# Kernel optimization log

Hardware: AMD Instinct MI355X
Metric: run time of the kernel (lower is better)

Reference implementation:

```python
import jax, jax.numpy as jnp
import numpy as np

N = 50000      # nodes
E = 800000     # edges (avg degree 16)
D = 3          # dim_world
L = 128        # latent_dim
STEPS = 10     # message passing steps
RID = 64       # num_rigid_ids
REMB = 16      # rigid_embedding_dim


def _mlp2(x, w1, b1, w2, b2):
    # 2-layer MLP: Linear -> ReLU -> Linear (layer_norm=False, dropout=0)
    return jnp.maximum(x @ w1 + b1, 0.0) @ w2 + b2


def setup_inputs() -> dict:
    key = jax.random.key(0)
    ks = jax.random.split(key, 24)
    f32 = jnp.float32

    def lin(k, i, o):
        return (jax.random.normal(k, (i, o), f32) / np.sqrt(i)).astype(f32)

    node_in = 2 * D + 1 + REMB   # 23
    edge_in = 2 * D + 2 + 1      # 9

    receivers = jax.random.randint(ks[4], (E,), 0, N)
    # no self edges (radius_graph uses include_self_edges=False)
    senders = (receivers + jax.random.randint(ks[3], (E,), 1, N)) % N

    inp = {
        'positions': jax.random.uniform(ks[0], (N, D), f32),
        'velocities': jax.random.normal(ks[1], (N, D), f32),
        'rigid_id': jax.random.randint(ks[2], (N,), 0, RID),
        'senders': senders,
        'receivers': receivers,
        'rigid_emb': jax.random.normal(ks[5], (RID, REMB), f32) * 0.1,
        # node encoder
        'ne_w1': lin(ks[6], node_in, L), 'ne_b1': jnp.zeros((L,), f32),
        'ne_w2': lin(ks[7], L, L),       'ne_b2': jnp.zeros((L,), f32),
        # edge encoder
        'ee_w1': lin(ks[8], edge_in, L), 'ee_b1': jnp.zeros((L,), f32),
        'ee_w2': lin(ks[9], L, L),       'ee_b2': jnp.zeros((L,), f32),
        # processor blocks (stacked over STEPS)
        'pe_w1': (jax.random.normal(ks[10], (STEPS, 3 * L, L), f32) / np.sqrt(3 * L)).astype(f32),
        'pe_b1': jnp.zeros((STEPS, L), f32),
        'pe_w2': (jax.random.normal(ks[11], (STEPS, L, L), f32) / np.sqrt(L)).astype(f32),
        'pe_b2': jnp.zeros((STEPS, L), f32),
        'pn_w1': (jax.random.normal(ks[12], (STEPS, 2 * L, L), f32) / np.sqrt(2 * L)).astype(f32),
        'pn_b1': jnp.zeros((STEPS, L), f32),
        'pn_w2': (jax.random.normal(ks[13], (STEPS, L, L), f32) / np.sqrt(L)).astype(f32),
        'pn_b2': jnp.zeros((STEPS, L), f32),
        # decoder (2 layers -> output_dim = D)
        'de_w1': lin(ks[14], L, L), 'de_b1': jnp.zeros((L,), f32),
        'de_w2': lin(ks[15], L, D), 'de_b2': jnp.zeros((D,), f32),
    }
    return inp


def reference(positions, velocities, rigid_id, senders, receivers, rigid_emb,
              ne_w1, ne_b1, ne_w2, ne_b2, ee_w1, ee_b1, ee_w2, ee_b2,
              pe_w1, pe_b1, pe_w2, pe_b2, pn_w1, pn_b1, pn_w2, pn_b2,
              de_w1, de_b1, de_w2, de_b2):
    n = positions.shape[0]
    dt = positions.dtype

    # ----- feature construction (build_gns_graph_inputs + rigid features) -----
    deg = jax.ops.segment_sum(jnp.ones(receivers.shape, dt), receivers, num_segments=n)[:, None]
    center = positions.mean(axis=0, keepdims=True)
    rigid_feat = rigid_emb[rigid_id]                                # [N, REMB]
    node_feat = jnp.concatenate([velocities, positions - center, deg, rigid_feat], axis=-1)

    rel_pos = positions[senders] - positions[receivers]             # [E, D]
    rel_vel = velocities[senders] - velocities[receivers]
    sq = jnp.sum(rel_pos * rel_pos, axis=-1, keepdims=True)
    dist = jnp.sqrt(sq)
    same = (rigid_id[senders] == rigid_id[receivers]).astype(dt)[:, None]
    edge_feat = jnp.concatenate([rel_pos, rel_vel, dist, sq, same], axis=-1)

    # ----- encode -----
    nl = _mlp2(node_feat, ne_w1, ne_b1, ne_w2, ne_b2)               # [N, L]
    el = _mlp2(edge_feat, ee_w1, ee_b1, ee_w2, ee_b2)               # [E, L]

    # ----- process: gather -> edge MLP -> scatter-add -> node MLP, residual -----
    for i in range(pe_w1.shape[0]):
        edge_in = jnp.concatenate([el, nl[senders], nl[receivers]], axis=-1)  # [E, 3L]
        el = el + _mlp2(edge_in, pe_w1[i], pe_b1[i], pe_w2[i], pe_b2[i])
        agg = jax.ops.segment_sum(el, receivers, num_segments=n)              # [N, L]
        node_in = jnp.concatenate([nl, agg], axis=-1)                         # [N, 2L]
        nl = nl + _mlp2(node_in, pn_w1[i], pn_b1[i], pn_w2[i], pn_b2[i])

    # ----- decode -----
    return _mlp2(nl, de_w1, de_b1, de_w2, de_b2)                    # [N, D]
```

## Files before the change

### kernel.cpp

```cpp
#include <hip/hip_runtime.h>
#include <hip/hip_bf16.h>

#define NN 50000
#define NE 800000
#define LDIM 128
#define NSTEPS 10

typedef __hip_bfloat16 bf16;
typedef __bf16 bf8v __attribute__((ext_vector_type(8)));
typedef float f4v __attribute__((ext_vector_type(4)));
typedef unsigned short u16x8 __attribute__((ext_vector_type(8)));

__device__ inline float bflo(unsigned int u) {
    union { unsigned int i; float f; } x; x.i = u << 16; return x.f;
}
__device__ inline float bfhi(unsigned int u) {
    union { unsigned int i; float f; } x; x.i = u & 0xffff0000u; return x.f;
}
__device__ inline unsigned short f2bf(float f) {
    __hip_bfloat16 h = __float2bfloat16(f);
    unsigned short u; __builtin_memcpy(&u, &h, 2); return u;
}

__device__ __forceinline__ void gl_lds16(const void* g, void* l) {
    __builtin_amdgcn_global_load_lds(
        (const __attribute__((address_space(1))) unsigned int*)g,
        (__attribute__((address_space(3))) unsigned int*)l, 16, 0, 0);
}


__global__ void k_hist(const int* __restrict__ rcv, int* __restrict__ cnt) {
    int i = blockIdx.x * 256 + threadIdx.x;
    if (i < NE) atomicAdd(&cnt[rcv[i]], 1);
}

__global__ __launch_bounds__(1024) void k_scan(
    const int* __restrict__ cnt, int* __restrict__ row_start,
    int* __restrict__ cur, float* __restrict__ degf) {
    __shared__ int part[1024];
    const int t = threadIdx.x;
    const int CH = (NN + 1023) / 1024;
    int b0 = t * CH, b1 = b0 + CH; if (b1 > NN) b1 = NN; if (b0 > NN) b0 = NN;
    int s = 0;
    for (int i = b0; i < b1; i++) s += cnt[i];
    part[t] = s;
    __syncthreads();
    for (int off = 1; off < 1024; off <<= 1) {
        int v = (t >= off) ? part[t - off] : 0;
        __syncthreads();
        part[t] += v;
        __syncthreads();
    }
    int run = part[t] - s;
    for (int i = b0; i < b1; i++) {
        row_start[i] = run; cur[i] = run; degf[i] = (float)cnt[i];
        run += cnt[i];
    }
    if (t == 1023) row_start[NN] = part[1023];
}

__global__ void k_scatter(const int* __restrict__ snd, const int* __restrict__ rcv,
                          int* __restrict__ cur,
                          unsigned short* __restrict__ snd_p, unsigned short* __restrict__ rcv_p) {
    int i = blockIdx.x * 256 + threadIdx.x;
    if (i < NE) {
        int r = rcv[i];
        int p = atomicAdd(&cur[r], 1);
        snd_p[p] = (unsigned short)snd[i];
        rcv_p[p] = (unsigned short)r;
    }
}

__global__ void k_center(const float* __restrict__ pos, float* __restrict__ csum) {
    __shared__ float s[3][256];
    float a = 0.f, b = 0.f, c = 0.f;
    for (int i = blockIdx.x * 256 + threadIdx.x; i < NN; i += gridDim.x * 256) {
        a += pos[3 * i]; b += pos[3 * i + 1]; c += pos[3 * i + 2];
    }
    int t = threadIdx.x;
    s[0][t] = a; s[1][t] = b; s[2][t] = c;
    __syncthreads();
    for (int off = 128; off > 0; off >>= 1) {
        if (t < off) {
            s[0][t] += s[0][t + off];
            s[1][t] += s[1][t + off];
            s[2][t] += s[2][t + off];
        }
        __syncthreads();
    }
    if (t == 0) {
        atomicAdd(&csum[0], s[0][0]);
        atomicAdd(&csum[1], s[1][0]);
        atomicAdd(&csum[2], s[2][0]);
    }
}


__global__ void k_prep_w(const float* __restrict__ w, unsigned short* __restrict__ wf,
                         int KT, int Ksrc, int lo) {
    int b = blockIdx.x;
    int s = b / (KT * 8), rem = b % (KT * 8);
    int kt = rem / 8, nt = rem % 8;
    int lane = threadIdx.x, col = lane & 15, quad = lane >> 4;
    const float* W = w + (size_t)s * Ksrc * 128;
    u16x8 o;
#pragma unroll
    for (int jj = 0; jj < 8; jj++) {
        int k = kt * 32 + quad * 8 + jj;
        float x = (k < Ksrc) ? W[(size_t)k * 128 + nt * 16 + col] : 0.f;
        unsigned short h = f2bf(x);
        if (lo) h = f2bf(x - bflo(h));
        o[jj] = h;
    }
    *(u16x8*)(wf + (((size_t)b) * 64 + lane) * 8) = o;
}


__global__ __launch_bounds__(256) void k_agg(
    const unsigned short* __restrict__ el, const int* __restrict__ row_start,
    unsigned short* __restrict__ agg) {
    const int wave = threadIdx.x >> 6, lane = threadIdx.x & 63;
    const int n = blockIdx.x * 4 + wave;
    if (n >= NN) return;
    const int sub = lane >> 4, c16 = lane & 15;
    const int st = row_start[n], en = row_start[n + 1];
    float s[8];
#pragma unroll
    for (int k = 0; k < 8; k++) s[k] = 0.f;
    for (int q = st + sub; q < en; q += 4) {
        uint4 v = *(const uint4*)(el + (size_t)q * 128 + c16 * 8);
        s[0] += bflo(v.x); s[1] += bfhi(v.x);
        s[2] += bflo(v.y); s[3] += bfhi(v.y);
        s[4] += bflo(v.z); s[5] += bfhi(v.z);
        s[6] += bflo(v.w); s[7] += bfhi(v.w);
    }
#pragma unroll
    for (int k = 0; k < 8; k++) {
        s[k] += __shfl_xor(s[k], 16);
        s[k] += __shfl_xor(s[k], 32);
    }
    if (sub == 0) {
        u16x8 o;
#pragma unroll
        for (int k = 0; k < 8; k++) o[k] = f2bf(s[k]);
        *(u16x8*)(agg + (size_t)n * 128 + c16 * 8) = o;
    }
}


__global__ __launch_bounds__(256) void k_node_enc_m(
    const float* __restrict__ pos, const float* __restrict__ vel,
    const int* __restrict__ rid, const float* __restrict__ remb,
    const float* __restrict__ degf, const float* __restrict__ csum,
    const unsigned short* __restrict__ w1h, const unsigned short* __restrict__ w1l,
    const float* __restrict__ b1,
    const unsigned short* __restrict__ w2h, const unsigned short* __restrict__ w2l,
    const float* __restrict__ b2,
    unsigned short* __restrict__ nlh, unsigned short* __restrict__ nll) {
    __shared__ __align__(16) unsigned short feat_s[32 * 72];
    __shared__ __align__(16) unsigned short hid_s[32 * 264];
    const int tid = threadIdx.x, wave = tid >> 6, lane = tid & 63;
    const int col = lane & 15, quad = lane >> 4;
    bf8v W1H[2], W1L[2], W2H[4][2], W2L[4][2];
#pragma unroll
    for (int t = 0; t < 2; t++) {
        W1H[t] = *(const bf8v*)(w1h + ((size_t)(2 * wave + t) * 64 + lane) * 8);
        W1L[t] = *(const bf8v*)(w1l + ((size_t)(2 * wave + t) * 64 + lane) * 8);
    }
#pragma unroll
    for (int kt = 0; kt < 4; kt++)
#pragma unroll
        for (int t = 0; t < 2; t++) {
            W2H[kt][t] = *(const bf8v*)(w2h + ((size_t)(kt * 8 + 2 * wave + t) * 64 + lane) * 8);
            W2L[kt][t] = *(const bf8v*)(w2l + ((size_t)(kt * 8 + 2 * wave + t) * 64 + lane) * 8);
        }
    float bias1[2], bias2[2];
#pragma unroll
    for (int t = 0; t < 2; t++) {
        bias1[t] = b1[(2 * wave + t) * 16 + col];
        bias2[t] = b2[(2 * wave + t) * 16 + col];
    }
    float cx = csum[0] * (1.0f / NN), cy = csum[1] * (1.0f / NN), cz = csum[2] * (1.0f / NN);
    uint4 z = {0u, 0u, 0u, 0u};
    for (int s2 = tid; s2 < 288; s2 += 256) *(uint4*)(feat_s + s2 * 8) = z;

    for (int it = 0; it < 4; it++) {
        const int base = blockIdx.x * 128 + it * 32;
        if (base >= NN) break;
        __syncthreads();
        if (tid < 32) {
            int n = base + tid; if (n > NN - 1) n = NN - 1;
            float v[23];
            v[0] = vel[3 * n]; v[1] = vel[3 * n + 1]; v[2] = vel[3 * n + 2];
            v[3] = pos[3 * n] - cx; v[4] = pos[3 * n + 1] - cy; v[5] = pos[3 * n + 2] - cz;
            v[6] = degf[n];
            int rb = rid[n] * 16;
#pragma unroll
            for (int k = 0; k < 16; k++) v[7 + k] = remb[rb + k];
            unsigned short* f = feat_s + tid * 72;
#pragma unroll
            for (int k = 0; k < 23; k++) {
                unsigned short h = f2bf(v[k]);
                f[k] = h; f[32 + k] = f2bf(v[k] - bflo(h));
            }
        }
        __syncthreads();
        f4v acc[2][2];
#pragma unroll
        for (int mt = 0; mt < 2; mt++)
#pragma unroll
            for (int t = 0; t < 2; t++) acc[mt][t] = (f4v){0.f, 0.f, 0.f, 0.f};
        {
            bf8v a0h = *(const bf8v*)(feat_s + col * 72 + quad * 8);
            bf8v a1h = *(const bf8v*)(feat_s + (16 + col) * 72 + quad * 8);
            bf8v a0l = *(const bf8v*)(feat_s + col * 72 + 32 + quad * 8);
            bf8v a1l = *(const bf8v*)(feat_s + (16 + col) * 72 + 32 + quad * 8);
#pragma unroll
            for (int t = 0; t < 2; t++) {
                acc[0][t] = __builtin_amdgcn_mfma_f32_16x16x32_bf16(a0h, W1H[t], acc[0][t], 0, 0, 0);
                acc[1][t] = __builtin_amdgcn_mfma_f32_16x16x32_bf16(a1h, W1H[t], acc[1][t], 0, 0, 0);
                acc[0][t] = __builtin_amdgcn_mfma_f32_16x16x32_bf16(a0l, W1H[t], acc[0][t], 0, 0, 0);
                acc[1][t] = __builtin_amdgcn_mfma_f32_16x16x32_bf16(a1l, W1H[t], acc[1][t], 0, 0, 0);
                acc[0][t] = __builtin_amdgcn_mfma_f32_16x16x32_bf16(a0h, W1L[t], acc[0][t], 0, 0, 0);
                acc[1][t] = __builtin_amdgcn_mfma_f32_16x16x32_bf16(a1h, W1L[t], acc[1][t], 0, 0, 0);
            }
        }
#pragma unroll
        for (int mt = 0; mt < 2; mt++)
#pragma unroll
// ... 121 lines not shown
        f4v acc[2][2];
#pragma unroll
        for (int mt = 0; mt < 2; mt++)
#pragma unroll
            for (int t = 0; t < 2; t++) acc[mt][t] = (f4v){0.f, 0.f, 0.f, 0.f};
        {
            bf8v a0h = *(const bf8v*)(feat_s + col * 72 + quad * 8);
            bf8v a1h = *(const bf8v*)(feat_s + (16 + col) * 72 + quad * 8);
            bf8v a0l = *(const bf8v*)(feat_s + col * 72 + 32 + quad * 8);
            bf8v a1l = *(const bf8v*)(feat_s + (16 + col) * 72 + 32 + quad * 8);
#pragma unroll
            for (int t = 0; t < 2; t++) {
                acc[0][t] = __builtin_amdgcn_mfma_f32_16x16x32_bf16(a0h, W1H[t], acc[0][t], 0, 0, 0);
                acc[1][t] = __builtin_amdgcn_mfma_f32_16x16x32_bf16(a1h, W1H[t], acc[1][t], 0, 0, 0);
                acc[0][t] = __builtin_amdgcn_mfma_f32_16x16x32_bf16(a0l, W1H[t], acc[0][t], 0, 0, 0);
                acc[1][t] = __builtin_amdgcn_mfma_f32_16x16x32_bf16(a1l, W1H[t], acc[1][t], 0, 0, 0);
                acc[0][t] = __builtin_amdgcn_mfma_f32_16x16x32_bf16(a0h, W1L[t], acc[0][t], 0, 0, 0);
                acc[1][t] = __builtin_amdgcn_mfma_f32_16x16x32_bf16(a1h, W1L[t], acc[1][t], 0, 0, 0);
            }
        }
#pragma unroll
        for (int mt = 0; mt < 2; mt++)
#pragma unroll
            for (int t = 0; t < 2; t++) {
                const int nc = (2 * wave + t) * 16 + col;
#pragma unroll
                for (int r = 0; r < 4; r++) {
                    float h = fmaxf(acc[mt][t][r] + bias1[t], 0.f);
                    unsigned short hh = f2bf(h);
                    hid_s[(mt * 16 + quad * 4 + r) * 264 + nc] = hh;
                    hid_s[(mt * 16 + quad * 4 + r) * 264 + 128 + nc] = f2bf(h - bflo(hh));
                }
            }
        __syncthreads();
#pragma unroll
        for (int mt = 0; mt < 2; mt++)
#pragma unroll
            for (int t = 0; t < 2; t++) acc[mt][t] = (f4v){0.f, 0.f, 0.f, 0.f};
#pragma unroll
        for (int kt = 0; kt < 8; kt++) {
            int w = kt & 3;
            bf8v a0 = *(const bf8v*)(hid_s + col * 264 + kt * 32 + quad * 8);
            bf8v a1 = *(const bf8v*)(hid_s + (16 + col) * 264 + kt * 32 + quad * 8);
#pragma unroll
            for (int t = 0; t < 2; t++) {
                acc[0][t] = __builtin_amdgcn_mfma_f32_16x16x32_bf16(a0, W2H[w][t], acc[0][t], 0, 0, 0);
                acc[1][t] = __builtin_amdgcn_mfma_f32_16x16x32_bf16(a1, W2H[w][t], acc[1][t], 0, 0, 0);
            }
        }
#pragma unroll
        for (int kt = 0; kt < 4; kt++) {
            bf8v a0 = *(const bf8v*)(hid_s + col * 264 + kt * 32 + quad * 8);
            bf8v a1 = *(const bf8v*)(hid_s + (16 + col) * 264 + kt * 32 + quad * 8);
#pragma unroll
            for (int t = 0; t < 2; t++) {
                acc[0][t] = __builtin_amdgcn_mfma_f32_16x16x32_bf16(a0, W2L[kt][t], acc[0][t], 0, 0, 0);
                acc[1][t] = __builtin_amdgcn_mfma_f32_16x16x32_bf16(a1, W2L[kt][t], acc[1][t], 0, 0, 0);
            }
        }
        __syncthreads();
#pragma unroll
        for (int mt = 0; mt < 2; mt++)
#pragma unroll
            for (int t = 0; t < 2; t++) {
                const int nc = (2 * wave + t) * 16 + col;
#pragma unroll
                for (int r = 0; r < 4; r++)
                    hid_s[(mt * 16 + quad * 4 + r) * 264 + nc] = f2bf(acc[mt][t][r] + bias2[t]);
            }
        __syncthreads();
#pragma unroll
        for (int p = 0; p < 2; p++) {
            int s2 = p * 256 + tid, e = s2 >> 4, c16 = s2 & 15;
            *(uint4*)(el + (size_t)(base + e) * 128 + c16 * 8) =
                *(const uint4*)(hid_s + e * 264 + c16 * 8);
        }
    }
}


__global__ __launch_bounds__(256) void k_edge_step(
    unsigned short* __restrict__ el, const unsigned short* __restrict__ nlh,
    const unsigned short* __restrict__ snd, const unsigned short* __restrict__ rcv,
    const unsigned short* __restrict__ w1f, const float* __restrict__ b1,
    const unsigned short* __restrict__ w2f, const float* __restrict__ b2) {
    __shared__ __align__(1024) unsigned short stage_s[2][3][32][128];
    __shared__ __align__(16) unsigned short hid_s[32 * 136];
    const int tid = threadIdx.x;
    const int wave = tid >> 6, lane = tid & 63;
    const int col = lane & 15, quad = lane >> 4;
    const int erow = tid >> 4, c16 = tid & 15;

    bf8v W1[12][2], W2[4][2];
#pragma unroll
    for (int kt = 0; kt < 12; kt++)
#pragma unroll
        for (int t = 0; t < 2; t++)
            W1[kt][t] = *(const bf8v*)(w1f + ((size_t)(kt * 8 + 2 * wave + t) * 64 + lane) * 8);
#pragma unroll
    for (int kt = 0; kt < 4; kt++)
#pragma unroll
        for (int t = 0; t < 2; t++)
            W2[kt][t] = *(const bf8v*)(w2f + ((size_t)(kt * 8 + 2 * wave + t) * 64 + lane) * 8);
    float bias1[2], bias2[2];
#pragma unroll
    for (int t = 0; t < 2; t++) {
        bias1[t] = b1[(2 * wave + t) * 16 + col];
        bias2[t] = b2[(2 * wave + t) * 16 + col];
    }

    const int srow0 = wave * 8 + (lane >> 4);
    const int srow1 = srow0 + 4;
    const int skb = (lane & 15) * 16;
    const int soff0 = skb ^ ((srow0 & 7) << 4);
    const int soff1 = skb ^ ((srow1 & 7) << 4);
    const int gb0 = blockIdx.x * 128;
    const char* elc = (const char*)el;
    const char* nlc = (const char*)nlh;

    auto issue = [&](int t, int b, int si0, int si1, int ri0, int ri1) {
        char* s0 = (char*)&stage_s[b][0][wave * 8][0];
        char* s1 = (char*)&stage_s[b][1][wave * 8][0];
        char* s2 = (char*)&stage_s[b][2][wave * 8][0];
        const size_t gb = (size_t)(gb0 + t * 32);
        gl_lds16(elc + (gb + srow0) * 256 + soff0, s0);
        gl_lds16(elc + (gb + srow1) * 256 + soff1, s0 + 1024);
        gl_lds16(nlc + (size_t)si0 * 256 + soff0, s1);
        gl_lds16(nlc + (size_t)si1 * 256 + soff1, s1 + 1024);
        gl_lds16(nlc + (size_t)ri0 * 256 + soff0, s2);
        gl_lds16(nlc + (size_t)ri1 * 256 + soff1, s2 + 1024);
    };

    {
        int si0 = snd[gb0 + srow0], si1 = snd[gb0 + srow1];
        int ri0 = rcv[gb0 + srow0], ri1 = rcv[gb0 + srow1];
        issue(0, 0, si0, si1, ri0, ri1);
    }
    int nsi0 = snd[gb0 + 32 + srow0], nsi1 = snd[gb0 + 32 + srow1];
    int nri0 = rcv[gb0 + 32 + srow0], nri1 = rcv[gb0 + 32 + srow1];

    for (int it = 0; it < 4; it++) {
        const int cur = it & 1, nxt = cur ^ 1;
        const int base = gb0 + it * 32;
        __syncthreads();
        if (it < 3) {
            issue(it + 1, nxt, nsi0, nsi1, nri0, nri1);
            if (it < 2) {
                int gb = gb0 + (it + 2) * 32;
                nsi0 = snd[gb + srow0]; nsi1 = snd[gb + srow1];
                nri0 = rcv[gb + srow0]; nri1 = rcv[gb + srow1];
            }
        }

        f4v acc[2][2];
#pragma unroll
        for (int mt = 0; mt < 2; mt++)
#pragma unroll
            for (int t = 0; t < 2; t++) acc[mt][t] = (f4v){0.f, 0.f, 0.f, 0.f};
        const int sw = (col & 7) << 4;
#pragma unroll
        for (int kt = 0; kt < 12; kt++) {
            const char* sb = (const char*)&stage_s[cur][kt >> 2][0][0];
            const int kb = (kt & 3) * 64 + quad * 16;
            bf8v a0 = *(const bf8v*)(sb + col * 256 + (kb ^ sw));
            bf8v a1 = *(const bf8v*)(sb + (16 + col) * 256 + (kb ^ sw));
            acc[0][0] = __builtin_amdgcn_mfma_f32_16x16x32_bf16(a0, W1[kt][0], acc[0][0], 0, 0, 0);
            acc[0][1] = __builtin_amdgcn_mfma_f32_16x16x32_bf16(a0, W1[kt][1], acc[0][1], 0, 0, 0);
            acc[1][0] = __builtin_amdgcn_mfma_f32_16x16x32_bf16(a1, W1[kt][0], acc[1][0], 0, 0, 0);
            acc[1][1] = __builtin_amdgcn_mfma_f32_16x16x32_bf16(a1, W1[kt][1], acc[1][1], 0, 0, 0);
        }
#pragma unroll
        for (int mt = 0; mt < 2; mt++)
#pragma unroll
            for (int t = 0; t < 2; t++) {
                const int nc = (2 * wave + t) * 16 + col;
#pragma unroll
                for (int r = 0; r < 4; r++) {
                    float v = fmaxf(acc[mt][t][r] + bias1[t], 0.f);
                    hid_s[(mt * 16 + quad * 4 + r) * 136 + nc] = f2bf(v);
                }
            }
        __syncthreads();

#pragma unroll
        for (int mt = 0; mt < 2; mt++)
#pragma unroll
            for (int t = 0; t < 2; t++) acc[mt][t] = (f4v){0.f, 0.f, 0.f, 0.f};
#pragma unroll
        for (int kt = 0; kt < 4; kt++) {
            bf8v a0 = *(const bf8v*)(hid_s + col * 136 + kt * 32 + quad * 8);
            bf8v a1 = *(const bf8v*)(hid_s + (16 + col) * 136 + kt * 32 + quad * 8);
            acc[0][0] = __builtin_amdgcn_mfma_f32_16x16x32_bf16(a0, W2[kt][0], acc[0][0], 0, 0, 0);
            acc[0][1] = __builtin_amdgcn_mfma_f32_16x16x32_bf16(a0, W2[kt][1], acc[0][1], 0, 0, 0);
            acc[1][0] = __builtin_amdgcn_mfma_f32_16x16x32_bf16(a1, W2[kt][0], acc[1][0], 0, 0, 0);
            acc[1][1] = __builtin_amdgcn_mfma_f32_16x16x32_bf16(a1, W2[kt][1], acc[1][1], 0, 0, 0);
        }
        __syncthreads();

#pragma unroll
        for (int mt = 0; mt < 2; mt++)
#pragma unroll
            for (int t = 0; t < 2; t++) {
                const int nc = (2 * wave + t) * 16 + col;
#pragma unroll
                for (int r = 0; r < 4; r++) {
                    const int row = mt * 16 + quad * 4 + r;
                    float res = bflo((unsigned int)stage_s[cur][0][row][nc ^ ((row & 7) << 3)]);
                    float v = acc[mt][t][r] + bias2[t] + res;
                    hid_s[row * 136 + nc] = f2bf(v);
                }
            }
        __syncthreads();
#pragma unroll
        for (int p = 0; p < 2; p++) {
            int e = p * 16 + erow;
            *(uint4*)(el + (size_t)(base + e) * 128 + c16 * 8) =
                *(const uint4*)(hid_s + e * 136 + c16 * 8);
        }
    }
}


__global__ __launch_bounds__(256) void k_node_step_s(
    unsigned short* __restrict__ nlh, unsigned short* __restrict__ nll,
    const unsigned short* __restrict__ agg,
    const unsigned short* __restrict__ w1h, const unsigned short* __restrict__ w1l,
    const float* __restrict__ b1,
    const unsigned short* __restrict__ w2h, const unsigned short* __restrict__ w2l,
    const float* __restrict__ b2) {
    __shared__ __align__(16) unsigned short a_s[32 * 392];
    __shared__ __align__(16) unsigned short hid_s[32 * 264];
    const int tid = threadIdx.x, wave = tid >> 6, lane = tid & 63;
    const int col = lane & 15, quad = lane >> 4;
    bf8v W1H[8][2], W1L[8][2], W2H[4][2], W2L[4][2];
#pragma unroll
    for (int kt = 0; kt < 8; kt++)
#pragma unroll
        for (int t = 0; t < 2; t++) {
            W1H[kt][t] = *(const bf8v*)(w1h + ((size_t)(kt * 8 + 2 * wave + t) * 64 + lane) * 8);
            W1L[kt][t] = *(const bf8v*)(w1l + ((size_t)(kt * 8 + 2 * wave + t) * 64 + lane) * 8);
        }
#pragma unroll
    for (int kt = 0; kt < 4; kt++)
#pragma unroll
        for (int t = 0; t < 2; t++) {
            W2H[kt][t] = *(const bf8v*)(w2h + ((size_t)(kt * 8 + 2 * wave + t) * 64 + lane) * 8);
            W2L[kt][t] = *(const bf8v*)(w2l + ((size_t)(kt * 8 + 2 * wave + t) * 64 + lane) * 8);
        }
    float bias1[2], bias2[2];
#pragma unroll
    for (int t = 0; t < 2; t++) {
        bias1[t] = b1[(2 * wave + t) * 16 + col];
        bias2[t] = b2[(2 * wave + t) * 16 + col];
    }
    for (int it = 0; it < 2; it++) {
        const int base = blockIdx.x * 64 + it * 32;
        if (base >= NN) break;
        __syncthreads();
#pragma unroll
        for (int p = 0; p < 2; p++) {
            int e = p * 16 + (tid >> 4), c16 = tid & 15;
            int n = base + e; if (n > NN - 1) n = NN - 1;
            *(uint4*)(a_s + e * 392 + c16 * 8) =
                *(const uint4*)(nlh + (size_t)n * 128 + c16 * 8);
            *(uint4*)(a_s + e * 392 + 128 + c16 * 8) =
                *(const uint4*)(nll + (size_t)n * 128 + c16 * 8);
            *(uint4*)(a_s + e * 392 + 256 + c16 * 8) =
                *(const uint4*)(agg + (size_t)n * 128 + c16 * 8);
        }
        __syncthreads();

        f4v acc[2][2];
#pragma unroll
        for (int mt = 0; mt < 2; mt++)
#pragma unroll
            for (int t = 0; t < 2; t++) acc[mt][t] = (f4v){0.f, 0.f, 0.f, 0.f};
#pragma unroll
        for (int kt = 0; kt < 8; kt++) {
            bf8v a0 = *(const bf8v*)(a_s + col * 392 + kt * 32 + quad * 8);
            bf8v a1 = *(const bf8v*)(a_s + (16 + col) * 392 + kt * 32 + quad * 8);
#pragma unroll
            for (int t = 0; t < 2; t++) {
                acc[0][t] = __builtin_amdgcn_mfma_f32_16x16x32_bf16(a0, W1H[kt & 3][t], acc[0][t], 0, 0, 0);
                acc[1][t] = __builtin_amdgcn_mfma_f32_16x16x32_bf16(a1, W1H[kt & 3][t], acc[1][t], 0, 0, 0);
            }
        }
#pragma unroll
        for (int kt = 0; kt < 4; kt++) {
            bf8v a0 = *(const bf8v*)(a_s + col * 392 + 256 + kt * 32 + quad * 8);
            bf8v a1 = *(const bf8v*)(a_s + (16 + col) * 392 + 256 + kt * 32 + quad * 8);
#pragma unroll
            for (int t = 0; t < 2; t++) {
                acc[0][t] = __builtin_amdgcn_mfma_f32_16x16x32_bf16(a0, W1H[4 + kt][t], acc[0][t], 0, 0, 0);
                acc[1][t] = __builtin_amdgcn_mfma_f32_16x16x32_bf16(a1, W1H[4 + kt][t], acc[1][t], 0, 0, 0);
            }
        }
#pragma unroll
        for (int kt = 0; kt < 4; kt++) {
            bf8v a0 = *(const bf8v*)(a_s + col * 392 + kt * 32 + quad * 8);
            bf8v a1 = *(const bf8v*)(a_s + (16 + col) * 392 + kt * 32 + quad * 8);
#pragma unroll
// ... 103 lines not shown
        float w[8];
#pragma unroll
        for (int t = 0; t < 8; t++) w[t] = w1[(kc * 8 + t) * 128 + j];
#pragma unroll
        for (int e = 0; e < 16; e++) {
            float4 h0 = *(const float4*)&inl[e][kc * 8];
            float4 h1 = *(const float4*)&inl[e][kc * 8 + 4];
            acc[e] = fmaf(h0.x, w[0], acc[e]); acc[e] = fmaf(h0.y, w[1], acc[e]);
            acc[e] = fmaf(h0.z, w[2], acc[e]); acc[e] = fmaf(h0.w, w[3], acc[e]);
            acc[e] = fmaf(h1.x, w[4], acc[e]); acc[e] = fmaf(h1.y, w[5], acc[e]);
            acc[e] = fmaf(h1.z, w[6], acc[e]); acc[e] = fmaf(h1.w, w[7], acc[e]);
        }
    }
#pragma unroll
    for (int e = 0; e < 16; e++) hid[e][j] = fmaxf(acc[e], 0.f);
    __syncthreads();
    if (j < 48) {
        int e = j / 3, ch = j - 3 * (j / 3);
        float s = b2[ch];
        for (int k = 0; k < 128; k++) s = fmaf(hid[e][k], w2[k * 3 + ch], s);
        out[(size_t)(base + e) * 3 + ch] = s;
    }
}


extern "C" void kernel_launch(void* const* d_in, const int* in_sizes, int n_in,
                              void* d_out, int out_size, void* d_ws, size_t ws_size,
                              hipStream_t stream) {
    (void)in_sizes; (void)n_in; (void)out_size; (void)ws_size;
    const float* pos   = (const float*)d_in[0];
    const float* vel   = (const float*)d_in[1];
    const int*   rid   = (const int*)d_in[2];
    const int*   snd   = (const int*)d_in[3];
    const int*   rcv   = (const int*)d_in[4];
    const float* remb  = (const float*)d_in[5];
    const float* ne_w1 = (const float*)d_in[6];
    const float* ne_b1 = (const float*)d_in[7];
    const float* ne_w2 = (const float*)d_in[8];
    const float* ne_b2 = (const float*)d_in[9];
    const float* ee_w1 = (const float*)d_in[10];
    const float* ee_b1 = (const float*)d_in[11];
    const float* ee_w2 = (const float*)d_in[12];
    const float* ee_b2 = (const float*)d_in[13];
    const float* pe_w1 = (const float*)d_in[14];
    const float* pe_b1 = (const float*)d_in[15];
    const float* pe_w2 = (const float*)d_in[16];
    const float* pe_b2 = (const float*)d_in[17];
    const float* pn_w1 = (const float*)d_in[18];
    const float* pn_b1 = (const float*)d_in[19];
    const float* pn_w2 = (const float*)d_in[20];
    const float* pn_b2 = (const float*)d_in[21];
    const float* de_w1 = (const float*)d_in[22];
    const float* de_b1 = (const float*)d_in[23];
    const float* de_w2 = (const float*)d_in[24];
    const float* de_b2 = (const float*)d_in[25];
    float* out = (float*)d_out;

    char* p = (char*)d_ws;
    auto carve = [&](size_t bytes) { void* q = (void*)p; p += (bytes + 15) & ~(size_t)15; return q; };
    unsigned short* el    = (unsigned short*)carve((size_t)NE * LDIM * 2);
    unsigned short* nlh   = (unsigned short*)carve((size_t)NN * LDIM * 2);
    unsigned short* nll   = (unsigned short*)carve((size_t)NN * LDIM * 2);
    unsigned short* agg   = (unsigned short*)carve((size_t)NN * LDIM * 2);
    unsigned short* w1f_e = (unsigned short*)carve((size_t)NSTEPS * 12 * 8 * 512 * 2);
    unsigned short* w2f_e = (unsigned short*)carve((size_t)NSTEPS * 4 * 8 * 512 * 2);
    unsigned short* w1h_n = (unsigned short*)carve((size_t)NSTEPS * 8 * 8 * 512 * 2);
    unsigned short* w1l_n = (unsigned short*)carve((size_t)NSTEPS * 8 * 8 * 512 * 2);
    unsigned short* w2h_n = (unsigned short*)carve((size_t)NSTEPS * 4 * 8 * 512 * 2);
    unsigned short* w2l_n = (unsigned short*)carve((size_t)NSTEPS * 4 * 8 * 512 * 2);
    unsigned short* eew1h = (unsigned short*)carve((size_t)1 * 8 * 512 * 2);
    unsigned short* eew1l = (unsigned short*)carve((size_t)1 * 8 * 512 * 2);
    unsigned short* eew2h = (unsigned short*)carve((size_t)4 * 8 * 512 * 2);
    unsigned short* eew2l = (unsigned short*)carve((size_t)4 * 8 * 512 * 2);
    unsigned short* new1h = (unsigned short*)carve((size_t)1 * 8 * 512 * 2);
    unsigned short* new1l = (unsigned short*)carve((size_t)1 * 8 * 512 * 2);
    unsigned short* new2h = (unsigned short*)carve((size_t)4 * 8 * 512 * 2);
    unsigned short* new2l = (unsigned short*)carve((size_t)4 * 8 * 512 * 2);
    unsigned short* snd_p = (unsigned short*)carve((size_t)NE * 2);
    unsigned short* rcv_p = (unsigned short*)carve((size_t)NE * 2);
    int*            rs    = (int*)carve((size_t)(NN + 1) * 4);
    int*            cnt   = (int*)carve((size_t)NN * 4);
    int*            cur   = (int*)carve((size_t)NN * 4);
    float*          degf  = (float*)carve((size_t)NN * 4);
    float*          csum  = (float*)carve(16);

    hipMemsetAsync(cnt, 0, (size_t)NN * 4, stream);
    hipMemsetAsync(csum, 0, 16, stream);
    k_hist<<<NE / 256, 256, 0, stream>>>(rcv, cnt);
    k_scan<<<1, 1024, 0, stream>>>(cnt, rs, cur, degf);
    k_center<<<64, 256, 0, stream>>>(pos, csum);
    k_scatter<<<NE / 256, 256, 0, stream>>>(snd, rcv, cur, snd_p, rcv_p);
    k_prep_w<<<NSTEPS * 12 * 8, 64, 0, stream>>>(pe_w1, w1f_e, 12, 384, 0);
    k_prep_w<<<NSTEPS * 4 * 8, 64, 0, stream>>>(pe_w2, w2f_e, 4, 128, 0);
    k_prep_w<<<NSTEPS * 8 * 8, 64, 0, stream>>>(pn_w1, w1h_n, 8, 256, 0);
    k_prep_w<<<NSTEPS * 8 * 8, 64, 0, stream>>>(pn_w1, w1l_n, 8, 256, 1);
    k_prep_w<<<NSTEPS * 4 * 8, 64, 0, stream>>>(pn_w2, w2h_n, 4, 128, 0);
    k_prep_w<<<NSTEPS * 4 * 8, 64, 0, stream>>>(pn_w2, w2l_n, 4, 128, 1);
    k_prep_w<<<8, 64, 0, stream>>>(ee_w1, eew1h, 1, 9, 0);
    k_prep_w<<<8, 64, 0, stream>>>(ee_w1, eew1l, 1, 9, 1);
    k_prep_w<<<4 * 8, 64, 0, stream>>>(ee_w2, eew2h, 4, 128, 0);
    k_prep_w<<<4 * 8, 64, 0, stream>>>(ee_w2, eew2l, 4, 128, 1);
    k_prep_w<<<8, 64, 0, stream>>>(ne_w1, new1h, 1, 23, 0);
    k_prep_w<<<8, 64, 0, stream>>>(ne_w1, new1l, 1, 23, 1);
    k_prep_w<<<4 * 8, 64, 0, stream>>>(ne_w2, new2h, 4, 128, 0);
    k_prep_w<<<4 * 8, 64, 0, stream>>>(ne_w2, new2l, 4, 128, 1);

    k_node_enc_m<<<(NN + 127) / 128, 256, 0, stream>>>(pos, vel, rid, remb, degf, csum,
                                                       new1h, new1l, ne_b1, new2h, new2l, ne_b2, nlh, nll);
    k_edge_enc_m<<<NE / 128, 256, 0, stream>>>(pos, vel, rid, snd_p, rcv_p,
                                               eew1h, eew1l, ee_b1, eew2h, eew2l, ee_b2, el);
    for (int i = 0; i < NSTEPS; i++) {
        k_edge_step<<<NE / 128, 256, 0, stream>>>(el, nlh, snd_p, rcv_p,
            w1f_e + (size_t)i * 12 * 8 * 512, pe_b1 + i * 128,
            w2f_e + (size_t)i * 4 * 8 * 512, pe_b2 + i * 128);
        k_agg<<<(NN + 3) / 4, 256, 0, stream>>>(el, rs, agg);
        k_node_step_s<<<(NN + 63) / 64, 256, 0, stream>>>(nlh, nll, agg,
            w1h_n + (size_t)i * 8 * 8 * 512, w1l_n + (size_t)i * 8 * 8 * 512, pn_b1 + i * 128,
            w2h_n + (size_t)i * 4 * 8 * 512, w2l_n + (size_t)i * 4 * 8 * 512, pn_b2 + i * 128);
    }
    k_decode<<<NN / 16, 128, 0, stream>>>(nlh, nll, de_w1, de_b1, de_w2, de_b2, out);
}
```

Before: 2.889 ms.

## Process one 32-edge tile per block in edge step, dropping in-block double buffering

The edge-step kernel now handles a single 32-edge tile per block instead of looping over four tiles with a double-buffered LDS stage, and it launches four times as many blocks. The gathers are issued before the per-thread weight registers are loaded, so the two overlap. This halves the LDS footprint, which may allow more resident blocks, and moves latency hiding from software pipelining to occupancy. In exchange, every block reloads the full weight set from global memory, which multiplies weight traffic by four.

```diff
diff --git a/kernel.cpp b/kernel.cpp
--- a/kernel.cpp
+++ b/kernel.cpp
@@ -434,139 +434,120 @@
     const unsigned short* __restrict__ snd, const unsigned short* __restrict__ rcv,
     const unsigned short* __restrict__ w1f, const float* __restrict__ b1,
     const unsigned short* __restrict__ w2f, const float* __restrict__ b2) {
-    __shared__ __align__(1024) unsigned short stage_s[2][3][32][128];
+    __shared__ __align__(1024) unsigned short stage_s[3][32][128];
     __shared__ __align__(16) unsigned short hid_s[32 * 136];
     const int tid = threadIdx.x;
     const int wave = tid >> 6, lane = tid & 63;
     const int col = lane & 15, quad = lane >> 4;
     const int erow = tid >> 4, c16 = tid & 15;
 
-    bf8v W1[12][2], W2[4][2];
-#pragma unroll
-    for (int kt = 0; kt < 12; kt++)
-#pragma unroll
-        for (int t = 0; t < 2; t++)
-            W1[kt][t] = *(const bf8v*)(w1f + ((size_t)(kt * 8 + 2 * wave + t) * 64 + lane) * 8);
-#pragma unroll
-    for (int kt = 0; kt < 4; kt++)
-#pragma unroll
-        for (int t = 0; t < 2; t++)
-            W2[kt][t] = *(const bf8v*)(w2f + ((size_t)(kt * 8 + 2 * wave + t) * 64 + lane) * 8);
-    float bias1[2], bias2[2];
-#pragma unroll
-    for (int t = 0; t < 2; t++) {
-        bias1[t] = b1[(2 * wave + t) * 16 + col];
-        bias2[t] = b2[(2 * wave + t) * 16 + col];
-    }
-
     const int srow0 = wave * 8 + (lane >> 4);
     const int srow1 = srow0 + 4;
     const int skb = (lane & 15) * 16;
     const int soff0 = skb ^ ((srow0 & 7) << 4);
     const int soff1 = skb ^ ((srow1 & 7) << 4);
-    const int gb0 = blockIdx.x * 128;
+    const int gb0 = blockIdx.x * 32;
     const char* elc = (const char*)el;
     const char* nlc = (const char*)nlh;
 
-    auto issue = [&](int t, int b, int si0, int si1, int ri0, int ri1) {
-        char* s0 = (char*)&stage_s[b][0][wave * 8][0];
-        char* s1 = (char*)&stage_s[b][1][wave * 8][0];
-        char* s2 = (char*)&stage_s[b][2][wave * 8][0];
-        const size_t gb = (size_t)(gb0 + t * 32);
-        gl_lds16(elc + (gb + srow0) * 256 + soff0, s0);
-        gl_lds16(elc + (gb + srow1) * 256 + soff1, s0 + 1024);
+    {
+        int si0 = snd[gb0 + srow0], si1 = snd[gb0 + srow1];
+        int ri0 = rcv[gb0 + srow0], ri1 = rcv[gb0 + srow1];
+        char* s0 = (char*)&stage_s[0][wave * 8][0];
+        char* s1 = (char*)&stage_s[1][wave * 8][0];
+        char* s2 = (char*)&stage_s[2][wave * 8][0];
+        gl_lds16(elc + (size_t)(gb0 + srow0) * 256 + soff0, s0);
+        gl_lds16(elc + (size_t)(gb0 + srow1) * 256 + soff1, s0 + 1024);
         gl_lds16(nlc + (size_t)si0 * 256 + soff0, s1);
         gl_lds16(nlc + (size_t)si1 * 256 + soff1, s1 + 1024);
         gl_lds16(nlc + (size_t)ri0 * 256 + soff0, s2);
         gl_lds16(nlc + (size_t)ri1 * 256 + soff1, s2 + 1024);
-    };
-
-    {
-        int si0 = snd[gb0 + srow0], si1 = snd[gb0 + srow1];
-        int ri0 = rcv[gb0 + srow0], ri1 = rcv[gb0 + srow1];
-        issue(0, 0, si0, si1, ri0, ri1);
-    }
-    int nsi0 = snd[gb0 + 32 + srow0], nsi1 = snd[gb0 + 32 + srow1];
-    int nri0 = rcv[gb0 + 32 + srow0], nri1 = rcv[gb0 + 32 + srow1];
-
-    for (int it = 0; it < 4; it++) {
-        const int cur = it & 1, nxt = cur ^ 1;
-        const int base = gb0 + it * 32;
-        __syncthreads();
-        if (it < 3) {
-            issue(it + 1, nxt, nsi0, nsi1, nri0, nri1);
-            if (it < 2) {
-                int gb = gb0 + (it + 2) * 32;
-                nsi0 = snd[gb + srow0]; nsi1 = snd[gb + srow1];
-                nri0 = rcv[gb + srow0]; nri1 = rcv[gb + srow1];
-            }
-        }
-
-        f4v acc[2][2];
-#pragma unroll
-        for (int mt = 0; mt < 2; mt++)
-#pragma unroll
-            for (int t = 0; t < 2; t++) acc[mt][t] = (f4v){0.f, 0.f, 0.f, 0.f};
-        const int sw = (col & 7) << 4;
-#pragma unroll
-        for (int kt = 0; kt < 12; kt++) {
-            const char* sb = (const char*)&stage_s[cur][kt >> 2][0][0];
-            const int kb = (kt & 3) * 64 + quad * 16;
-            bf8v a0 = *(const bf8v*)(sb + col * 256 + (kb ^ sw));
-            bf8v a1 = *(const bf8v*)(sb + (16 + col) * 256 + (kb ^ sw));
-            acc[0][0] = __builtin_amdgcn_mfma_f32_16x16x32_bf16(a0, W1[kt][0], acc[0][0], 0, 0, 0);
-            acc[0][1] = __builtin_amdgcn_mfma_f32_16x16x32_bf16(a0, W1[kt][1], acc[0][1], 0, 0, 0);
-            acc[1][0] = __builtin_amdgcn_mfma_f32_16x16x32_bf16(a1, W1[kt][0], acc[1][0], 0, 0, 0);
-            acc[1][1] = __builtin_amdgcn_mfma_f32_16x16x32_bf16(a1, W1[kt][1], acc[1][1], 0, 0, 0);
-        }
-#pragma unroll
-        for (int mt = 0; mt < 2; mt++)
-#pragma unroll
-            for (int t = 0; t < 2; t++) {
-                const int nc = (2 * wave + t) * 16 + col;
-#pragma unroll
-                for (int r = 0; r < 4; r++) {
-                    float v = fmaxf(acc[mt][t][r] + bias1[t], 0.f);
-                    hid_s[(mt * 16 + quad * 4 + r) * 136 + nc] = f2bf(v);
-                }
-            }
-        __syncthreads();
-
-#pragma unroll
-        for (int mt = 0; mt < 2; mt++)
-#pragma unroll
-            for (int t = 0; t < 2; t++) acc[mt][t] = (f4v){0.f, 0.f, 0.f, 0.f};
-#pragma unroll
-        for (int kt = 0; kt < 4; kt++) {
-            bf8v a0 = *(const bf8v*)(hid_s + col * 136 + kt * 32 + quad * 8);
-            bf8v a1 = *(const bf8v*)(hid_s + (16 + col) * 136 + kt * 32 + quad * 8);
-            acc[0][0] = __builtin_amdgcn_mfma_f32_16x16x32_bf16(a0, W2[kt][0], acc[0][0], 0, 0, 0);
-            acc[0][1] = __builtin_amdgcn_mfma_f32_16x16x32_bf16(a0, W2[kt][1], acc[0][1], 0, 0, 0);
-            acc[1][0] = __builtin_amdgcn_mfma_f32_16x16x32_bf16(a1, W2[kt][0], acc[1][0], 0, 0, 0);
-            acc[1][1] = __builtin_amdgcn_mfma_f32_16x16x32_bf16(a1, W2[kt][1], acc[1][1], 0, 0, 0);
-        }
-        __syncthreads();
-
-#pragma unroll
-        for (int mt = 0; mt < 2; mt++)
-#pragma unroll
-            for (int t = 0; t < 2; t++) {
-                const int nc = (2 * wave + t) * 16 + col;
-#pragma unroll
-                for (int r = 0; r < 4; r++) {
-                    const int row = mt * 16 + quad * 4 + r;
-                    float res = bflo((unsigned int)stage_s[cur][0][row][nc ^ ((row & 7) << 3)]);
-                    float v = acc[mt][t][r] + bias2[t] + res;
-                    hid_s[row * 136 + nc] = f2bf(v);
-                }
-            }
-        __syncthreads();
-#pragma unroll
-        for (int p = 0; p < 2; p++) {
-            int e = p * 16 + erow;
-            *(uint4*)(el + (size_t)(base + e) * 128 + c16 * 8) =
-                *(const uint4*)(hid_s + e * 136 + c16 * 8);
-        }
+    }
+
+    bf8v W1[12][2], W2[4][2];
+#pragma unroll
+    for (int kt = 0; kt < 12; kt++)
+#pragma unroll
+        for (int t = 0; t < 2; t++)
+            W1[kt][t] = *(const bf8v*)(w1f + ((size_t)(kt * 8 + 2 * wave + t) * 64 + lane) * 8);
+#pragma unroll
+    for (int kt = 0; kt < 4; kt++)
+#pragma unroll
+        for (int t = 0; t < 2; t++)
+            W2[kt][t] = *(const bf8v*)(w2f + ((size_t)(kt * 8 + 2 * wave + t) * 64 + lane) * 8);
+    float bias1[2], bias2[2];
+#pragma unroll
+    for (int t = 0; t < 2; t++) {
+        bias1[t] = b1[(2 * wave + t) * 16 + col];
+        bias2[t] = b2[(2 * wave + t) * 16 + col];
+    }
+
+    __syncthreads();
+
+    f4v acc[2][2];
+#pragma unroll
+    for (int mt = 0; mt < 2; mt++)
+#pragma unroll
+        for (int t = 0; t < 2; t++) acc[mt][t] = (f4v){0.f, 0.f, 0.f, 0.f};
+    const int sw = (col & 7) << 4;
+#pragma unroll
+    for (int kt = 0; kt < 12; kt++) {
+        const char* sb = (const char*)&stage_s[kt >> 2][0][0];
+        const int kb = (kt & 3) * 64 + quad * 16;
+        bf8v a0 = *(const bf8v*)(sb + col * 256 + (kb ^ sw));
+        bf8v a1 = *(const bf8v*)(sb + (16 + col) * 256 + (kb ^ sw));
+        acc[0][0] = __builtin_amdgcn_mfma_f32_16x16x32_bf16(a0, W1[kt][0], acc[0][0], 0, 0, 0);
+        acc[0][1] = __builtin_amdgcn_mfma_f32_16x16x32_bf16(a0, W1[kt][1], acc[0][1], 0, 0, 0);
+        acc[1][0] = __builtin_amdgcn_mfma_f32_16x16x32_bf16(a1, W1[kt][0], acc[1][0], 0, 0, 0);
+        acc[1][1] = __builtin_amdgcn_mfma_f32_16x16x32_bf16(a1, W1[kt][1], acc[1][1], 0, 0, 0);
+    }
+#pragma unroll
+    for (int mt = 0; mt < 2; mt++)
+#pragma unroll
+        for (int t = 0; t < 2; t++) {
+            const int nc = (2 * wave + t) * 16 + col;
+#pragma unroll
+            for (int r = 0; r < 4; r++) {
+                float v = fmaxf(acc[mt][t][r] + bias1[t], 0.f);
+                hid_s[(mt * 16 + quad * 4 + r) * 136 + nc] = f2bf(v);
+            }
+        }
+    __syncthreads();
+
+#pragma unroll
+    for (int mt = 0; mt < 2; mt++)
+#pragma unroll
+        for (int t = 0; t < 2; t++) acc[mt][t] = (f4v){0.f, 0.f, 0.f, 0.f};
+#pragma unroll
+    for (int kt = 0; kt < 4; kt++) {
+        bf8v a0 = *(const bf8v*)(hid_s + col * 136 + kt * 32 + quad * 8);
+        bf8v a1 = *(const bf8v*)(hid_s + (16 + col) * 136 + kt * 32 + quad * 8);
+        acc[0][0] = __builtin_amdgcn_mfma_f32_16x16x32_bf16(a0, W2[kt][0], acc[0][0], 0, 0, 0);
+        acc[0][1] = __builtin_amdgcn_mfma_f32_16x16x32_bf16(a0, W2[kt][1], acc[0][1], 0, 0, 0);
+        acc[1][0] = __builtin_amdgcn_mfma_f32_16x16x32_bf16(a1, W2[kt][0], acc[1][0], 0, 0, 0);
+        acc[1][1] = __builtin_amdgcn_mfma_f32_16x16x32_bf16(a1, W2[kt][1], acc[1][1], 0, 0, 0);
+    }
+    __syncthreads();
+
+#pragma unroll
+    for (int mt = 0; mt < 2; mt++)
+#pragma unroll
+        for (int t = 0; t < 2; t++) {
+            const int nc = (2 * wave + t) * 16 + col;
+#pragma unroll
+            for (int r = 0; r < 4; r++) {
+                const int row = mt * 16 + quad * 4 + r;
+                float res = bflo((unsigned int)stage_s[0][row][nc ^ ((row & 7) << 3)]);
+                float v = acc[mt][t][r] + bias2[t] + res;
+                hid_s[row * 136 + nc] = f2bf(v);
+            }
+        }
+    __syncthreads();
+#pragma unroll
+    for (int p = 0; p < 2; p++) {
+        int e = p * 16 + erow;
+        *(uint4*)(el + (size_t)(gb0 + e) * 128 + c16 * 8) =
+            *(const uint4*)(hid_s + e * 136 + c16 * 8);
     }
 }
 
@@ -864,7 +845,7 @@
     k_edge_enc_m<<<NE / 128, 256, 0, stream>>>(pos, vel, rid, snd_p, rcv_p,
                                                eew1h, eew1l, ee_b1, eew2h, eew2l, ee_b2, el);
     for (int i = 0; i < NSTEPS; i++) {
-        k_edge_step<<<NE / 128, 256, 0, stream>>>(el, nlh, snd_p, rcv_p,
+        k_edge_step<<<NE / 32, 256, 0, stream>>>(el, nlh, snd_p, rcv_p,
             w1f_e + (size_t)i * 12 * 8 * 512, pe_b1 + i * 128,
             w2f_e + (size_t)i * 4 * 8 * 512, pe_b2 + i * 128);
         k_agg<<<(NN + 3) / 4, 256, 0, stream>>>(el, rs, agg);
```

New measurement: 2.912 ms. No clear change (+0.8%).

## Fuse segment-sum aggregation into edge step via node-aligned edge blocks

Applied to the files above, without the earlier changes.

Removes the separate k_agg kernel. Each edge_step block now owns a contiguous, node-aligned range of receiver-sorted edges, found through a first_node table built during the scan, and accumulates the per-node sums of the new edge latents directly from shared memory into agg. This drops a full re-read of the edge latent array and one launch per step. In exchange, block workloads become variable in size, the aggregation is a serial loop over rows run by only half the threads, and fewer edges may be processed per block when receivers span block boundaries.

```diff
diff --git a/kernel.cpp b/kernel.cpp
--- a/kernel.cpp
+++ b/kernel.cpp
@@ -5,6 +5,7 @@
 #define NE 800000
 #define LDIM 128
 #define NSTEPS 10
+#define NB (NE / 128)
 
 typedef __hip_bfloat16 bf16;
 typedef __bf16 bf8v __attribute__((ext_vector_type(8)));
@@ -36,7 +37,7 @@
 
 __global__ __launch_bounds__(1024) void k_scan(
     const int* __restrict__ cnt, int* __restrict__ row_start,
-    int* __restrict__ cur, float* __restrict__ degf) {
+    int* __restrict__ cur, float* __restrict__ degf, int* __restrict__ first_node) {
     __shared__ int part[1024];
     const int t = threadIdx.x;
     const int CH = (NN + 1023) / 1024;
@@ -54,9 +55,10 @@
     int run = part[t] - s;
     for (int i = b0; i < b1; i++) {
         row_start[i] = run; cur[i] = run; degf[i] = (float)cnt[i];
+        if (run < NE) atomicMin(&first_node[run >> 7], i);
         run += cnt[i];
     }
-    if (t == 1023) row_start[NN] = part[1023];
+    if (t == 1023) { row_start[NN] = part[1023]; first_node[NB] = NN; }
 }
 
 __global__ void k_scatter(const int* __restrict__ snd, const int* __restrict__ rcv,
@@ -113,38 +115,6 @@
         o[jj] = h;
     }
     *(u16x8*)(wf + (((size_t)b) * 64 + lane) * 8) = o;
-}
-
-
-__global__ __launch_bounds__(256) void k_agg(
-    const unsigned short* __restrict__ el, const int* __restrict__ row_start,
-    unsigned short* __restrict__ agg) {
-    const int wave = threadIdx.x >> 6, lane = threadIdx.x & 63;
-    const int n = blockIdx.x * 4 + wave;
-    if (n >= NN) return;
-    const int sub = lane >> 4, c16 = lane & 15;
-    const int st = row_start[n], en = row_start[n + 1];
-    float s[8];
-#pragma unroll
-    for (int k = 0; k < 8; k++) s[k] = 0.f;
-    for (int q = st + sub; q < en; q += 4) {
-        uint4 v = *(const uint4*)(el + (size_t)q * 128 + c16 * 8);
-        s[0] += bflo(v.x); s[1] += bfhi(v.x);
-        s[2] += bflo(v.y); s[3] += bfhi(v.y);
-        s[4] += bflo(v.z); s[5] += bfhi(v.z);
-        s[6] += bflo(v.w); s[7] += bfhi(v.w);
-    }
-#pragma unroll
-    for (int k = 0; k < 8; k++) {
-        s[k] += __shfl_xor(s[k], 16);
-        s[k] += __shfl_xor(s[k], 32);
-    }
-    if (sub == 0) {
-        u16x8 o;
-#pragma unroll
-        for (int k = 0; k < 8; k++) o[k] = f2bf(s[k]);
-        *(u16x8*)(agg + (size_t)n * 128 + c16 * 8) = o;
-    }
 }
 
 
@@ -432,14 +402,22 @@
 __global__ __launch_bounds__(256) void k_edge_step(
     unsigned short* __restrict__ el, const unsigned short* __restrict__ nlh,
     const unsigned short* __restrict__ snd, const unsigned short* __restrict__ rcv,
+    const int* __restrict__ rs, const int* __restrict__ first_node,
     const unsigned short* __restrict__ w1f, const float* __restrict__ b1,
-    const unsigned short* __restrict__ w2f, const float* __restrict__ b2) {
+    const unsigned short* __restrict__ w2f, const float* __restrict__ b2,
+    unsigned short* __restrict__ agg) {
     __shared__ __align__(1024) unsigned short stage_s[2][3][32][128];
     __shared__ __align__(16) unsigned short hid_s[32 * 136];
+    __shared__ int rcv_s[32];
     const int tid = threadIdx.x;
     const int wave = tid >> 6, lane = tid & 63;
     const int col = lane & 15, quad = lane >> 4;
     const int erow = tid >> 4, c16 = tid & 15;
+
+    const int n0 = first_node[blockIdx.x];
+    const int n1 = first_node[blockIdx.x + 1];
+    const int st = rs[n0], en = rs[n1];
+    const int nt = (en - st + 31) >> 5;
 
     bf8v W1[12][2], W2[4][2];
 #pragma unroll
@@ -464,17 +442,17 @@
     const int skb = (lane & 15) * 16;
     const int soff0 = skb ^ ((srow0 & 7) << 4);
     const int soff1 = skb ^ ((srow1 & 7) << 4);
-    const int gb0 = blockIdx.x * 128;
     const char* elc = (const char*)el;
     const char* nlc = (const char*)nlh;
 
+    auto clampe = [&](int e) { return e < en ? e : en - 1; };
     auto issue = [&](int t, int b, int si0, int si1, int ri0, int ri1) {
         char* s0 = (char*)&stage_s[b][0][wave * 8][0];
         char* s1 = (char*)&stage_s[b][1][wave * 8][0];
         char* s2 = (char*)&stage_s[b][2][wave * 8][0];
-        const size_t gb = (size_t)(gb0 + t * 32);
-        gl_lds16(elc + (gb + srow0) * 256 + soff0, s0);
-        gl_lds16(elc + (gb + srow1) * 256 + soff1, s0 + 1024);
+        const int gb = st + t * 32;
+        gl_lds16(elc + (size_t)clampe(gb + srow0) * 256 + soff0, s0);
+        gl_lds16(elc + (size_t)clampe(gb + srow1) * 256 + soff1, s0 + 1024);
         gl_lds16(nlc + (size_t)si0 * 256 + soff0, s1);
         gl_lds16(nlc + (size_t)si1 * 256 + soff1, s1 + 1024);
         gl_lds16(nlc + (size_t)ri0 * 256 + soff0, s2);
@@ -482,23 +460,30 @@
     };
 
     {
-        int si0 = snd[gb0 + srow0], si1 = snd[gb0 + srow1];
-        int ri0 = rcv[gb0 + srow0], ri1 = rcv[gb0 + srow1];
+        int si0 = snd[clampe(st + srow0)], si1 = snd[clampe(st + srow1)];
+        int ri0 = rcv[clampe(st + srow0)], ri1 = rcv[clampe(st + srow1)];
         issue(0, 0, si0, si1, ri0, ri1);
     }
-    int nsi0 = snd[gb0 + 32 + srow0], nsi1 = snd[gb0 + 32 + srow1];
-    int nri0 = rcv[gb0 + 32 + srow0], nri1 = rcv[gb0 + 32 + srow1];
-
-    for (int it = 0; it < 4; it++) {
+    int nsi0 = 0, nsi1 = 0, nri0 = 0, nri1 = 0;
+    if (nt > 1) {
+        nsi0 = snd[clampe(st + 32 + srow0)]; nsi1 = snd[clampe(st + 32 + srow1)];
+        nri0 = rcv[clampe(st + 32 + srow0)]; nri1 = rcv[clampe(st + 32 + srow1)];
+    }
+
+    int curn = n0, cnt4 = 0;
+    float p0 = 0.f, p1 = 0.f, p2 = 0.f, p3 = 0.f;
+
+    for (int it = 0; it < nt; it++) {
         const int cur = it & 1, nxt = cur ^ 1;
-        const int base = gb0 + it * 32;
-        __syncthreads();
-        if (it < 3) {
+        const int base = st + it * 32;
+        __syncthreads();
+        if (tid < 32) rcv_s[tid] = rcv[clampe(base + tid)];
+        if (it + 1 < nt) {
             issue(it + 1, nxt, nsi0, nsi1, nri0, nri1);
-            if (it < 2) {
-                int gb = gb0 + (it + 2) * 32;
-                nsi0 = snd[gb + srow0]; nsi1 = snd[gb + srow1];
-                nri0 = rcv[gb + srow0]; nri1 = rcv[gb + srow1];
+            if (it + 2 < nt) {
+                int gb = st + (it + 2) * 32;
+                nsi0 = snd[clampe(gb + srow0)]; nsi1 = snd[clampe(gb + srow1)];
+                nri0 = rcv[clampe(gb + srow0)]; nri1 = rcv[clampe(gb + srow1)];
             }
         }
 
@@ -561,12 +546,39 @@
                 }
             }
         __syncthreads();
+
 #pragma unroll
         for (int p = 0; p < 2; p++) {
             int e = p * 16 + erow;
-            *(uint4*)(el + (size_t)(base + e) * 128 + c16 * 8) =
-                *(const uint4*)(hid_s + e * 136 + c16 * 8);
-        }
+            if (base + e < en)
+                *(uint4*)(el + (size_t)(base + e) * 128 + c16 * 8) =
+                    *(const uint4*)(hid_s + e * 136 + c16 * 8);
+        }
+
+        if (tid < 128) {
+            int rows = en - base; if (rows > 32) rows = 32;
+            for (int r = 0; r < rows; ++r) {
+                int nd = rcv_s[r];
+                if (nd != curn) {
+                    agg[(size_t)curn * 128 + tid] = f2bf((p0 + p1) + (p2 + p3));
+                    for (int m = curn + 1; m < nd; ++m)
+                        agg[(size_t)m * 128 + tid] = 0;
+                    curn = nd; p0 = p1 = p2 = p3 = 0.f; cnt4 = 0;
+                }
+                float v = bflo((unsigned int)hid_s[r * 136 + tid]);
+                switch (cnt4 & 3) {
+                    case 0: p0 += v; break;
+                    case 1: p1 += v; break;
+                    case 2: p2 += v; break;
+                    default: p3 += v; break;
+                }
+                cnt4++;
+            }
+        }
+    }
+    if (tid < 128) {
+        agg[(size_t)curn * 128 + tid] = f2bf((p0 + p1) + (p2 + p3));
+        for (int m = curn + 1; m < n1; ++m) agg[(size_t)m * 128 + tid] = 0;
     }
 }
 
@@ -836,12 +848,14 @@
     int*            cnt   = (int*)carve((size_t)NN * 4);
     int*            cur   = (int*)carve((size_t)NN * 4);
     float*          degf  = (float*)carve((size_t)NN * 4);
+    int*            fn    = (int*)carve((size_t)(NB + 1) * 4);
     float*          csum  = (float*)carve(16);
 
     hipMemsetAsync(cnt, 0, (size_t)NN * 4, stream);
     hipMemsetAsync(csum, 0, 16, stream);
+    hipMemsetAsync(fn, 0x7f, (size_t)(NB + 1) * 4, stream);
     k_hist<<<NE / 256, 256, 0, stream>>>(rcv, cnt);
-    k_scan<<<1, 1024, 0, stream>>>(cnt, rs, cur, degf);
+    k_scan<<<1, 1024, 0, stream>>>(cnt, rs, cur, degf, fn);
     k_center<<<64, 256, 0, stream>>>(pos, csum);
     k_scatter<<<NE / 256, 256, 0, stream>>>(snd, rcv, cur, snd_p, rcv_p);
     k_prep_w<<<NSTEPS * 12 * 8, 64, 0, stream>>>(pe_w1, w1f_e, 12, 384, 0);
@@ -864,10 +878,9 @@
     k_edge_enc_m<<<NE / 128, 256, 0, stream>>>(pos, vel, rid, snd_p, rcv_p,
                                                eew1h, eew1l, ee_b1, eew2h, eew2l, ee_b2, el);
     for (int i = 0; i < NSTEPS; i++) {
-        k_edge_step<<<NE / 128, 256, 0, stream>>>(el, nlh, snd_p, rcv_p,
+        k_edge_step<<<NB, 256, 0, stream>>>(el, nlh, snd_p, rcv_p, rs, fn,
             w1f_e + (size_t)i * 12 * 8 * 512, pe_b1 + i * 128,
-            w2f_e + (size_t)i * 4 * 8 * 512, pe_b2 + i * 128);
-        k_agg<<<(NN + 3) / 4, 256, 0, stream>>>(el, rs, agg);
+            w2f_e + (size_t)i * 4 * 8 * 512, pe_b2 + i * 128, agg);
         k_node_step_s<<<(NN + 63) / 64, 256, 0, stream>>>(nlh, nll, agg,
             w1h_n + (size_t)i * 8 * 8 * 512, w1l_n + (size_t)i * 8 * 8 * 512, pn_b1 + i * 128,
             w2h_n + (size_t)i * 4 * 8 * 512, w2l_n + (size_t)i * 4 * 8 * 512, pn_b2 + i * 128);
```

New measurement: 5.127 ms. 1.77x slower.
